# Performance work log

Measured on AMD Instinct MI355X. Metric: run time of the kernel, lower is better.

Reference implementation:

```python
import jax, jax.numpy as jnp
import numpy as np

# RRFU config (matches init_kwargs)
S = 2          # scale_factor
G = 4          # groups
K = 3          # sample_k
C = 64         # in_channels
B, H, W_IN = 4, 128, 128
SC = S * S     # s_c
KC = K * K     # sample_c (3x3 = 9)


def setup_inputs() -> dict:
    key = jax.random.key(0)
    ks = jax.random.split(key, 9)
    x = jax.random.normal(ks[0], (B, C, H, W_IN), jnp.float32)
    # 1x1 conv weights stored as (out_ch, in_ch); std chosen per module's init
    # (mask convs are zero-init in the original; use small random so math is nontrivial)
    w_off = jax.random.normal(ks[1], (G * SC * 2, C), jnp.float32) * 0.001
    b_off = jnp.zeros((G * SC * 2,), jnp.float32)
    w_offm = jax.random.normal(ks[2], (G * SC * 2, C), jnp.float32) * 0.01
    b_offm = jnp.zeros((G * SC * 2,), jnp.float32)
    w_sk = jax.random.normal(ks[3], (KC, C), jnp.float32) * 0.005
    b_sk = jnp.zeros((KC,), jnp.float32)
    w_km = jax.random.normal(ks[4], (KC, C), jnp.float32) * 0.01
    b_km = jnp.zeros((KC,), jnp.float32)
    return {"x": x, "w_off": w_off, "b_off": b_off, "w_offm": w_offm,
            "b_offm": b_offm, "w_sk": w_sk, "b_sk": b_sk, "w_km": w_km, "b_km": b_km}


def _conv1x1(x, w, b):
    return jnp.einsum('oc,bchw->bohw', w, x) + b[None, :, None, None]


def _bilinear_border(img, iy, ix):
    """img: (Cg,H,W); iy,ix: (Ho,Wo) pixel coords. grid_sample bilinear, padding_mode='border'."""
    Hh, Ww = img.shape[1], img.shape[2]
    ix = jnp.clip(ix, 0.0, Ww - 1.0)
    iy = jnp.clip(iy, 0.0, Hh - 1.0)
    x0 = jnp.floor(ix)
    y0 = jnp.floor(iy)
    wx = ix - x0
    wy = iy - y0
    x0i = x0.astype(jnp.int32)
    y0i = y0.astype(jnp.int32)
    x1i = jnp.minimum(x0i + 1, Ww - 1)
    y1i = jnp.minimum(y0i + 1, Hh - 1)
    v00 = img[:, y0i, x0i]
    v01 = img[:, y0i, x1i]
    v10 = img[:, y1i, x0i]
    v11 = img[:, y1i, x1i]
    return (v00 * (1 - wx) * (1 - wy) + v01 * wx * (1 - wy)
            + v10 * (1 - wx) * wy + v11 * wx * wy)


def reference(x, w_off, b_off, w_offm, b_offm, w_sk, b_sk, w_km, b_km):
    b0, c0, h0, w0 = x.shape
    # learned offsets, gated by sigmoid mask
    off = _conv1x1(x, w_off, b_off) * jax.nn.sigmoid(_conv1x1(x, w_offm, b_offm))
    bg = b0 * G
    # (b, g*S*S*2, h, w) -> (bg, S, S, 2, h, w) -> (bg, h, S, w, S, 2) -> (bg, S*h, S*w, 2)
    off = off.reshape(bg, S, S, 2, h0, w0).transpose(0, 4, 1, 5, 2, 3).reshape(bg, S * h0, S * w0, 2)
    Ho, Wo = S * h0, S * w0
    # coord_base + offset, normalized then un-normalized for align_corners=False grid_sample
    cx = jnp.arange(Wo, dtype=x.dtype) + 0.5
    cy = jnp.arange(Ho, dtype=x.dtype) + 0.5
    ix = (cx[None, None, :] + off[..., 0]) * (w0 / Wo) - 0.5  # (bg, Ho, Wo)
    iy = (cy[None, :, None] + off[..., 1]) * (h0 / Ho) - 0.5
    x_r = x.reshape(bg, c0 // G, h0, w0)
    x_def = jax.vmap(_bilinear_border)(x_r, iy, ix).reshape(b0, c0, Ho, Wo)
    # CARAFE-style dynamic reassembly: softmax kernel over 3x3 neighborhood
    sk = _conv1x1(x_def, w_sk, b_sk) * jax.nn.sigmoid(_conv1x1(x_def, w_km, b_km))
    skn = jax.nn.softmax(sk, axis=1)  # (b, 9, Ho, Wo)
    pad = K // 2
    xp = jnp.pad(x_def, ((0, 0), (0, 0), (pad, pad), (pad, pad)))  # zero pad like F.unfold
    out = jnp.zeros_like(x_def)
    for ky in range(K):  # fixed 3x3 taps; avoids materializing (b,c,9,Ho,Wo)
        for kx in range(K):
            out = out + skn[:, ky * K + kx][:, None] * xp[:, :, ky:ky + Ho, kx:kx + Wo]
    return out
```

## Files before the change

### kernel.cpp

```cpp
#include <hip/hip_runtime.h>
#include <hip/hip_fp16.h>

typedef _Float16 h2 __attribute__((ext_vector_type(2)));

constexpr int Bc  = 4;
constexpr int Cc  = 64;
constexpr int H0  = 128;
constexpr int W0  = 128;
constexpr int HW  = H0 * W0;
constexpr int Gc  = 4;
constexpr int HOc = H0 * 2;
constexpr int WOc = W0 * 2;

constexpr int TW = 16;
constexpr int TH = 8;
constexpr int HX = TW + 2;
constexpr int HY = TH + 2;
constexpr int NHALO = HX * HY;
constexpr int NTASK = Gc * NHALO;

constexpr int SXC = 10;
constexpr int SYC = 6;
constexpr int SN  = SXC * SYC;
constexpr int NPAIR = Cc / 2;
constexpr int NSTG  = NPAIR * SN;

union hu32 { unsigned u; h2 h; };

__device__ __forceinline__ float dot2(h2 a, unsigned bw, float c) {
    hu32 cv; cv.u = bw;
#if __has_builtin(__builtin_amdgcn_fdot2)
    return __builtin_amdgcn_fdot2(a, cv.h, c, false);
#else
    return fmaf((float)a[0], (float)cv.h[0],
                fmaf((float)a[1], (float)cv.h[1], c));
#endif
}

__global__ __launch_bounds__(256) void kT_prep(
    const float* __restrict__ w_off, const float* __restrict__ w_offm,
    const float* __restrict__ w_sk,  const float* __restrict__ w_km,
    __half2* __restrict__ wpk0, __half2* __restrict__ wpk)
{
    const int i = blockIdx.x * 256 + threadIdx.x;
    if (i < 2048) {
        const int c2  = i >> 6;
        const int rem = i & 63;
        const int mat = rem >> 5;
        const int r   = rem & 31;
        const float* src = mat ? w_offm : w_off;
        wpk0[i] = __floats2half2_rn(src[r * Cc + 2 * c2],
                                    src[r * Cc + 2 * c2 + 1]);
    } else if (i < 2048 + 576) {
        const int j   = i - 2048;
        const int mat = j >= 288;
        const int jj  = mat ? j - 288 : j;
        const int k   = jj >> 5;
        const int c2  = jj & 31;
        const float* src = mat ? w_km : w_sk;
        wpk[j] = __floats2half2_rn(src[k * Cc + 2 * c2],
                                   src[k * Cc + 2 * c2 + 1]);
    }
}

__global__ __launch_bounds__(256) void k0_offsets(
    const float* __restrict__ x, const unsigned* __restrict__ wpk0,
    const float* __restrict__ b_off, const float* __restrict__ b_offm,
    __half2* __restrict__ offbuf, unsigned* __restrict__ xt)
{
    const int b    = blockIdx.y;
    const int t    = threadIdx.x;
    const int wave = t >> 6, lane = t & 63;
    const int r0   = __builtin_amdgcn_readfirstlane(wave * 8);
    const int px   = blockIdx.x * 64 + lane;

    float a[8], m[8];
#pragma unroll
    for (int q = 0; q < 8; ++q) { a[q] = 0.f; m[q] = 0.f; }
    unsigned xtr[NPAIR];

    const float*    xp = x + (size_t)b * Cc * HW + px;
    const unsigned* wp = wpk0 + r0;

#pragma unroll 4
    for (int c2 = 0; c2 < NPAIR; ++c2) {
        const float x0 = xp[(2 * c2)     * HW];
        const float x1 = xp[(2 * c2 + 1) * HW];
        hu32 xh; xh.h = h2{(_Float16)x0, (_Float16)x1};
        xtr[c2] = xh.u;
#pragma unroll
        for (int q = 0; q < 8; ++q) {
            a[q] = dot2(xh.h, wp[c2 * 64 + q],      a[q]);
            m[q] = dot2(xh.h, wp[c2 * 64 + 32 + q], m[q]);
        }
    }

    __half2* ob = offbuf + ((size_t)b * HW + px) * 16 + (r0 >> 1);
#pragma unroll
    for (int j = 0; j < 4; ++j) {
        const int r = r0 + 2 * j;
        const float sx = 1.f / (1.f + __expf(-(m[2 * j]     + b_offm[r])));
        const float sy = 1.f / (1.f + __expf(-(m[2 * j + 1] + b_offm[r + 1])));
        const float vx = (a[2 * j]     + b_off[r])     * sx;
        const float vy = (a[2 * j + 1] + b_off[r + 1]) * sy;
        ob[j] = __floats2half2_rn(vx, vy);
    }

    if (wave == 0) {
        unsigned* xo = xt + ((size_t)b * HW + px) * NPAIR;
#pragma unroll
        for (int c2 = 0; c2 < NPAIR; ++c2) xo[c2] = xtr[c2];
    }
}

__global__ __launch_bounds__(256) void k1_fused(
    const unsigned* __restrict__ xt, const __half2* __restrict__ offbuf,
    const unsigned* __restrict__ wsku, const float* __restrict__ b_sk,
    const float* __restrict__ b_km,
    float* __restrict__ out)
{
    __shared__ h2       xd2[NPAIR][NHALO];
    __shared__ unsigned xs_u[NSTG];
    __shared__ unsigned short kmbh[128 * 9];
    __shared__ unsigned sknb[128 * 9];

    const unsigned* wkmu = wsku + 288;

    const int b    = blockIdx.y;
    const int tp   = blockIdx.x;
    const int ox = (tp & 15) * TW;
    const int oyb = (tp >> 4) * (2 * TH);
    const int t  = threadIdx.x;
    const int sxr = (ox >> 1) - 1;
    const int syr0 = (oyb >> 1) - 1;
    const int syr1 = syr0 + (TH >> 1);

    const unsigned* xtb = xt + (size_t)b * HW * NPAIR;
    const __half2*  obb = offbuf + (size_t)b * HW * 16;

    unsigned pre0[8], pre1[8];
#pragma unroll
    for (int k = 0; k < 8; ++k) {
        const int i = t + k * 256;
        if (i < NSTG) {
            const int c2  = i & 31;
            const int pos = i >> 5;
            const int r   = pos / SXC;
            const int j   = pos - r * SXC;
            const int xx  = min(max(sxr + j, 0), W0 - 1);
            const int yy0 = min(max(syr0 + r, 0), H0 - 1);
            const int yy1 = min(max(syr1 + r, 0), H0 - 1);
            pre0[k] = xtb[(yy0 * W0 + xx) * NPAIR + c2];
            pre1[k] = xtb[(yy1 * W0 + xx) * NPAIR + c2];
        }
    }
#pragma unroll
    for (int k = 0; k < 8; ++k) {
        const int i = t + k * 256;
        if (i < NSTG) {
            const int c2 = i & 31, pos = i >> 5;
            xs_u[c2 * SN + pos] = pre0[k];
        }
    }
    __syncthreads();

    for (int yt = 0; yt < 2; ++yt) {
        const int oy  = oyb + yt * TH;
        const int syr = yt ? syr1 : syr0;
        const h2* xstage2 = (const h2*)xs_u;

        for (int task = t; task < NTASK; task += 256) {
            const int g   = task / NHALO;
            const int pix = task - g * NHALO;
            const int hy  = pix / HX;
            const int hx  = pix - hy * HX;
            const int gy  = oy - 1 + hy;
            const int gx  = ox - 1 + hx;
            if (gy < 0 || gy >= HOc || gx < 0 || gx >= WOc) {
#pragma unroll
                for (int p = 0; p < 8; ++p) xd2[g * 8 + p][pix] = (h2)0;
                continue;
            }
            const int sy = gy & 1, sx = gx & 1;
            const int h  = gy >> 1, w  = gx >> 1;
            const __half2 o2 = obb[(size_t)(h * W0 + w) * 16 + g * 4 + sy * 2 + sx];
            const float offx = __low2float(o2);
            const float offy = __high2float(o2);

            float ix = ((float)gx + 0.5f + offx) * 0.5f - 0.5f;
            float iy = ((float)gy + 0.5f + offy) * 0.5f - 0.5f;
            ix = fminf(fmaxf(ix, 0.f), (float)(W0 - 1));
            iy = fminf(fmaxf(iy, 0.f), (float)(H0 - 1));
            const float x0f = floorf(ix), y0f = floorf(iy);
            const float wx = ix - x0f,   wy = iy - y0f;
            const int x0 = (int)x0f, y0 = (int)y0f;
            const int x1 = min(x0 + 1, W0 - 1), y1 = min(y0 + 1, H0 - 1);
            const float w00 = (1.f - wx) * (1.f - wy);
            const float w01 = wx * (1.f - wy);
            const float w10 = (1.f - wx) * wy;
            const float w11 = wx * wy;

            const int j0 = x0 - sxr, j1 = x1 - sxr;
            const int i0 = y0 - syr, i1 = y1 - syr;
            const bool inl = (j0 >= 0) & (j1 < SXC) & (i0 >= 0) & (i1 < SYC);

            const _Float16 W00 = (_Float16)w00, W01 = (_Float16)w01;
            const _Float16 W10 = (_Float16)w10, W11 = (_Float16)w11;

            if (inl) {
                const int o00 = i0 * SXC + j0, o01 = i0 * SXC + j1;
                const int o10 = i1 * SXC + j0, o11 = i1 * SXC + j1;
                const h2* s2 = xstage2 + (g * 8) * SN;
#pragma unroll
                for (int p = 0; p < 8; ++p) {
                    const h2* pc = s2 + p * SN;
                    xd2[g * 8 + p][pix] =
                        pc[o00] * W00 + pc[o01] * W01 + pc[o10] * W10 + pc[o11] * W11;
                }
            } else {
                const int o00 = (y0 * W0 + x0) * NPAIR, o01 = (y0 * W0 + x1) * NPAIR;
                const int o10 = (y1 * W0 + x0) * NPAIR, o11 = (y1 * W0 + x1) * NPAIR;
#pragma unroll
                for (int p = 0; p < 8; ++p) {
                    const int c2 = g * 8 + p;
                    hu32 v00, v01, v10, v11;
                    v00.u = xtb[o00 + c2]; v01.u = xtb[o01 + c2];
                    v10.u = xtb[o10 + c2]; v11.u = xtb[o11 + c2];
                    xd2[c2][pix] =
                        v00.h * W00 + v01.h * W01 + v10.h * W10 + v11.h * W11;
                }
            }
        }
        __syncthreads();

        if (yt == 0) {
#pragma unroll
            for (int k = 0; k < 8; ++k) {
                const int i = t + k * 256;
                if (i < NSTG) {
                    const int c2 = i & 31, pos = i >> 5;
                    xs_u[c2 * SN + pos] = pre1[k];
                }
            }
        }

        {
            const int p   = t & 127;
            const int ctr = ((p >> 4) + 1) * HX + (p & 15) + 1;
            h2 xv[NPAIR];
#pragma unroll
            for (int c2 = 0; c2 < NPAIR; ++c2) xv[c2] = xd2[c2][ctr];

            float acc[9];
            if (t < 128) {
#pragma unroll
                for (int k = 0; k < 9; ++k) {
                    float a = 0.f;
#pragma unroll
                    for (int c2 = 0; c2 < NPAIR; ++c2)
                        a = dot2(xv[c2], wsku[k * 32 + c2], a);
                    acc[k] = a;
                }
            } else {
#pragma unroll
                for (int k = 0; k < 9; ++k) {
                    float a = 0.f;
#pragma unroll
                    for (int c2 = 0; c2 < NPAIR; ++c2)
                        a = dot2(xv[c2], wkmu[k * 32 + c2], a);
                    kmbh[p * 9 + k] = __half_as_ushort(__float2half(a));
                }
            }
            __syncthreads();

            if (t < 128) {
                float sv[9], mx = -1e30f;
#pragma unroll
                for (int k = 0; k < 9; ++k) {
                    const float z = __half2float(__ushort_as_half(kmbh[p * 9 + k]))
                                    + b_km[k];
                    sv[k] = (acc[k] + b_sk[k]) / (1.f + __expf(-z));
                    mx = fmaxf(mx, sv[k]);
                }
                float sum = 0.f;
#pragma unroll
                for (int k = 0; k < 9; ++k) { sv[k] = __expf(sv[k] - mx); sum += sv[k]; }
                const float inv = 1.f / sum;
#pragma unroll
                for (int k = 0; k < 9; ++k) {
                    const unsigned hu = __half_as_ushort(__float2half(sv[k] * inv));
                    sknb[p * 9 + k] = hu | (hu << 16);
                }
            }
        }
        __syncthreads();

        {
            const int sq    = t & 31;
            const int chunk = t >> 5;
            const int sqx = sq & 7, sqy = sq >> 3;
            const int hx0 = 2 * sqx, hy0 = 2 * sqy;
            const int p00 = (2 * sqy) * TW + 2 * sqx;

            hu32 s00[9], s01[9], s10[9], s11[9];
#pragma unroll
            for (int k = 0; k < 9; ++k) {
                s00[k].u = sknb[p00 * 9 + k];        s01[k].u = sknb[(p00 + 1) * 9 + k];
                s10[k].u = sknb[(p00 + TW) * 9 + k]; s11[k].u = sknb[(p00 + TW + 1) * 9 + k];
            }
            const int orow0 = oy + 2 * sqy, ocol0 = ox + 2 * sqx;

#pragma unroll
            for (int i = 0; i < 4; ++i) {
                const int pr = chunk * 4 + i;
                h2 wd[4][4];
#pragma unroll
                for (int ry = 0; ry < 4; ++ry) {
                    const int base = (hy0 + ry) * HX + hx0;
#pragma unroll
                    for (int rx = 0; rx < 4; ++rx)
                        wd[ry][rx] = xd2[pr][base + rx];
                }
                h2 a00 = (h2)0, a01 = (h2)0, a10 = (h2)0, a11 = (h2)0;
#pragma unroll
                for (int ky = 0; ky < 3; ++ky)
#pragma unroll
                    for (int kx = 0; kx < 3; ++kx) {
                        const int k = ky * 3 + kx;
                        a00 += s00[k].h * wd[ky    ][kx    ];
                        a01 += s01[k].h * wd[ky    ][kx + 1];
                        a10 += s10[k].h * wd[ky + 1][kx    ];
                        a11 += s11[k].h * wd[ky + 1][kx + 1];
                    }
                float* ob0 = out + ((size_t)(b * Cc + 2 * pr)) * (HOc * WOc)
                                 + (size_t)orow0 * WOc + ocol0;
                float* ob1 = ob0 + (size_t)(HOc * WOc);
                *reinterpret_cast<float2*>(ob0)       = make_float2((float)a00[0], (float)a01[0]);
                *reinterpret_cast<float2*>(ob0 + WOc) = make_float2((float)a10[0], (float)a11[0]);
                *reinterpret_cast<float2*>(ob1)       = make_float2((float)a00[1], (float)a01[1]);
                *reinterpret_cast<float2*>(ob1 + WOc) = make_float2((float)a10[1], (float)a11[1]);
            }
        }
        __syncthreads();
    }
}

extern "C" void kernel_launch(void* const* d_in, const int* in_sizes, int n_in,
                              void* d_out, int out_size, void* d_ws, size_t ws_size,
                              hipStream_t stream)
{
    const float* x      = (const float*)d_in[0];
    const float* w_off  = (const float*)d_in[1];
    const float* b_off  = (const float*)d_in[2];
    const float* w_offm = (const float*)d_in[3];
    const float* b_offm = (const float*)d_in[4];
    const float* w_sk   = (const float*)d_in[5];
    const float* b_sk   = (const float*)d_in[6];
    const float* w_km   = (const float*)d_in[7];
    const float* b_km   = (const float*)d_in[8];
    float* outp = (float*)d_out;

    const size_t off_bytes  = (size_t)Bc * HW * 16 * sizeof(__half2);
    const size_t xt_bytes   = (size_t)Bc * HW * NPAIR * sizeof(unsigned);
    const size_t wpk0_bytes = 2048 * sizeof(__half2);
    const size_t wpk_bytes  = 576 * sizeof(__half2);
    if (ws_size < off_bytes + xt_bytes + wpk0_bytes + wpk_bytes) return;
    __half2*  offbuf = (__half2*)d_ws;
    unsigned* xtbuf  = (unsigned*)((char*)d_ws + off_bytes);
    __half2*  wpk0   = (__half2*)((char*)d_ws + off_bytes + xt_bytes);
    __half2*  wpk    = (__half2*)((char*)d_ws + off_bytes + xt_bytes + wpk0_bytes);

    dim3 blk(256);
    hipLaunchKernelGGL(kT_prep, dim3(11), blk, 0, stream,
                       w_off, w_offm, w_sk, w_km, wpk0, wpk);

    dim3 g0(HW / 64, Bc);
    hipLaunchKernelGGL(k0_offsets, g0, blk, 0, stream,
                       x, (const unsigned*)wpk0, b_off, b_offm, offbuf, xtbuf);

    dim3 g1(256, Bc);
    hipLaunchKernelGGL(k1_fused, g1, blk, 0, stream,
                       xtbuf, offbuf, (const unsigned*)wpk, b_sk, b_km, outp);
}
```

Measured before the change: 55.43 us.

## Coalesce k0 stores via LDS transpose and prefetch offsets in k1

k0 now stages the fp16-packed x values and the per-pixel offsets in shared memory and writes them to global memory as contiguous coalesced words. Previously each lane wrote its own strided 128-byte and 64-byte rows. k1 loads the offsets for both row tiles up front into registers, alongside the existing xt prefetch, so the offset loads are no longer serialized inside the sampling loop. This adds shared memory and a block barrier to k0, and more live registers in k1.

Measured after the change: 59.54 us. 7.4% more time.

```diff
diff --git a/kernel.cpp b/kernel.cpp
--- a/kernel.cpp
+++ b/kernel.cpp
@@ -66,8 +66,11 @@
 __global__ __launch_bounds__(256) void k0_offsets(
     const float* __restrict__ x, const unsigned* __restrict__ wpk0,
     const float* __restrict__ b_off, const float* __restrict__ b_offm,
-    __half2* __restrict__ offbuf, unsigned* __restrict__ xt)
+    unsigned* __restrict__ offbuf, unsigned* __restrict__ xt)
 {
+    __shared__ unsigned xt_lds[64 * 33];
+    __shared__ unsigned ob_lds[64 * 17];
+
     const int b    = blockIdx.y;
     const int t    = threadIdx.x;
     const int wave = t >> 6, lane = t & 63;
@@ -77,7 +80,6 @@
     float a[8], m[8];
 #pragma unroll
     for (int q = 0; q < 8; ++q) { a[q] = 0.f; m[q] = 0.f; }
-    unsigned xtr[NPAIR];
 
     const float*    xp = x + (size_t)b * Cc * HW + px;
     const unsigned* wp = wpk0 + r0;
@@ -87,7 +89,7 @@
         const float x0 = xp[(2 * c2)     * HW];
         const float x1 = xp[(2 * c2 + 1) * HW];
         hu32 xh; xh.h = h2{(_Float16)x0, (_Float16)x1};
-        xtr[c2] = xh.u;
+        if (wave == 0) xt_lds[lane * 33 + c2] = xh.u;
 #pragma unroll
         for (int q = 0; q < 8; ++q) {
             a[q] = dot2(xh.h, wp[c2 * 64 + q],      a[q]);
@@ -95,7 +97,6 @@
         }
     }
 
-    __half2* ob = offbuf + ((size_t)b * HW + px) * 16 + (r0 >> 1);
 #pragma unroll
     for (int j = 0; j < 4; ++j) {
         const int r = r0 + 2 * j;
@@ -103,18 +104,28 @@
         const float sy = 1.f / (1.f + __expf(-(m[2 * j + 1] + b_offm[r + 1])));
         const float vx = (a[2 * j]     + b_off[r])     * sx;
         const float vy = (a[2 * j + 1] + b_off[r + 1]) * sy;
-        ob[j] = __floats2half2_rn(vx, vy);
-    }
-
-    if (wave == 0) {
-        unsigned* xo = xt + ((size_t)b * HW + px) * NPAIR;
-#pragma unroll
-        for (int c2 = 0; c2 < NPAIR; ++c2) xo[c2] = xtr[c2];
+        const __half2 hh = __floats2half2_rn(vx, vy);
+        union { __half2 h; unsigned u; } cv; cv.h = hh;
+        ob_lds[lane * 17 + (r0 >> 1) + j] = cv.u;
+    }
+    __syncthreads();
+
+    unsigned* xo = xt + ((size_t)b * HW + blockIdx.x * 64) * NPAIR;
+#pragma unroll
+    for (int it = 0; it < 8; ++it) {
+        const int idx = it * 256 + t;
+        xo[idx] = xt_lds[(idx >> 5) * 33 + (idx & 31)];
+    }
+    unsigned* oo = offbuf + ((size_t)b * HW + blockIdx.x * 64) * 16;
+#pragma unroll
+    for (int it = 0; it < 4; ++it) {
+        const int idx = it * 256 + t;
+        oo[idx] = ob_lds[(idx >> 4) * 17 + (idx & 15)];
     }
 }
 
 __global__ __launch_bounds__(256) void k1_fused(
-    const unsigned* __restrict__ xt, const __half2* __restrict__ offbuf,
+    const unsigned* __restrict__ xt, const unsigned* __restrict__ offbuf,
     const unsigned* __restrict__ wsku, const float* __restrict__ b_sk,
     const float* __restrict__ b_km,
     float* __restrict__ out)
@@ -136,7 +147,7 @@
     const int syr1 = syr0 + (TH >> 1);
 
     const unsigned* xtb = xt + (size_t)b * HW * NPAIR;
-    const __half2*  obb = offbuf + (size_t)b * HW * 16;
+    const unsigned* obu = offbuf + (size_t)b * HW * 16;
 
     unsigned pre0[8], pre1[8];
 #pragma unroll
@@ -154,6 +165,29 @@
             pre1[k] = xtb[(yy1 * W0 + xx) * NPAIR + c2];
         }
     }
+    unsigned o2p0[3] = {0u, 0u, 0u}, o2p1[3] = {0u, 0u, 0u};
+#pragma unroll
+    for (int it = 0; it < 3; ++it) {
+        const int task = t + it * 256;
+        if (task < NTASK) {
+            const int g   = task / NHALO;
+            const int pix = task - g * NHALO;
+            const int hy  = pix / HX;
+            const int hx  = pix - hy * HX;
+            const int gx  = ox - 1 + hx;
+            const int gy0 = oyb - 1 + hy;
+            const int gy1 = gy0 + TH;
+            if (gx >= 0 && gx < WOc) {
+                const int w = gx >> 1, sxb = gx & 1;
+                if (gy0 >= 0 && gy0 < HOc)
+                    o2p0[it] = obu[((gy0 >> 1) * W0 + w) * 16
+                                   + g * 4 + (gy0 & 1) * 2 + sxb];
+                if (gy1 < HOc)
+                    o2p1[it] = obu[((gy1 >> 1) * W0 + w) * 16
+                                   + g * 4 + (gy1 & 1) * 2 + sxb];
+            }
+        }
+    }
 #pragma unroll
     for (int k = 0; k < 8; ++k) {
         const int i = t + k * 256;
@@ -169,7 +203,10 @@
         const int syr = yt ? syr1 : syr0;
         const h2* xstage2 = (const h2*)xs_u;
 
-        for (int task = t; task < NTASK; task += 256) {
+#pragma unroll
+        for (int it = 0; it < 3; ++it) {
+            const int task = t + it * 256;
+            if (task >= NTASK) continue;
             const int g   = task / NHALO;
             const int pix = task - g * NHALO;
             const int hy  = pix / HX;
@@ -181,11 +218,9 @@
                 for (int p = 0; p < 8; ++p) xd2[g * 8 + p][pix] = (h2)0;
                 continue;
             }
-            const int sy = gy & 1, sx = gx & 1;
-            const int h  = gy >> 1, w  = gx >> 1;
-            const __half2 o2 = obb[(size_t)(h * W0 + w) * 16 + g * 4 + sy * 2 + sx];
-            const float offx = __low2float(o2);
-            const float offy = __high2float(o2);
+            hu32 o2u; o2u.u = yt ? o2p1[it] : o2p0[it];
+            const float offx = (float)o2u.h[0];
+            const float offy = (float)o2u.h[1];
 
             float ix = ((float)gx + 0.5f + offx) * 0.5f - 0.5f;
             float iy = ((float)gy + 0.5f + offy) * 0.5f - 0.5f;
@@ -360,12 +395,12 @@
     const float* b_km   = (const float*)d_in[8];
     float* outp = (float*)d_out;
 
-    const size_t off_bytes  = (size_t)Bc * HW * 16 * sizeof(__half2);
+    const size_t off_bytes  = (size_t)Bc * HW * 16 * sizeof(unsigned);
     const size_t xt_bytes   = (size_t)Bc * HW * NPAIR * sizeof(unsigned);
     const size_t wpk0_bytes = 2048 * sizeof(__half2);
     const size_t wpk_bytes  = 576 * sizeof(__half2);
     if (ws_size < off_bytes + xt_bytes + wpk0_bytes + wpk_bytes) return;
-    __half2*  offbuf = (__half2*)d_ws;
+    unsigned* offbuf = (unsigned*)d_ws;
     unsigned* xtbuf  = (unsigned*)((char*)d_ws + off_bytes);
     __half2*  wpk0   = (__half2*)((char*)d_ws + off_bytes + xt_bytes);
     __half2*  wpk    = (__half2*)((char*)d_ws + off_bytes + xt_bytes + wpk0_bytes);
```
